# Kernel tuning notes

Measured on AMD Instinct MI355X. Metric: run time of the kernel, lower is better.

The kernel has to match this reference:

```python
import jax, jax.numpy as jnp
import numpy as np

LAM = 20.0      # Sinkhorn entropic sharpness (exp(-LAM*M))
N_ITERS = 20    # fixed Sinkhorn iterations
EPS = 1e-8


def setup_inputs() -> dict:
    key = jax.random.key(0)
    k1, k2, k3, k4 = jax.random.split(key, 4)
    n, l, h, hid = 16, 256, 128, 128
    f = jax.random.normal(k1, (n, l, l, h), dtype=jnp.float32) * 0.1
    head = jax.random.uniform(k2, (n, l, l), dtype=jnp.float32)
    W1 = jax.random.normal(k3, (h, hid), dtype=jnp.float32) * (1.0 / np.sqrt(h))
    b1 = jnp.zeros((hid,), dtype=jnp.float32)
    W2 = jax.random.normal(k4, (hid, 1), dtype=jnp.float32) * (1.0 / np.sqrt(hid))
    b2 = jnp.zeros((1,), dtype=jnp.float32)
    return {"f": f, "head": head, "W1": W1, "b1": b1, "W2": W2, "b2": b2}


def _sinkhorn_loss(r, c, M):
    # r, c: (l,) histograms; M: (l, l) ground cost. Frogner-style Wasserstein loss.
    K = jnp.exp(-LAM * M)
    KM = K * M
    u0 = jnp.full_like(r, 1.0 / r.shape[0])

    def body(u, _):
        u = r / (K @ (c / (K.T @ u + EPS)) + EPS)
        return u, None

    u, _ = jax.lax.scan(body, u0, None, length=N_ITERS)
    v = c / (K.T @ u + EPS)
    return jnp.sum(u * (KM @ v))


def reference(f, head, W1, b1, W2, b2):
    n, l, _, h = f.shape
    # dense 2-layer MLP over every (i,j) arc feature -> scalar score
    hdn = jnp.tanh(f.reshape(n, l * l, h) @ W1 + b1)          # (n, l*l, hid)
    scores = (hdn @ W2 + b2).reshape(n, l, l)                  # (n, l, l)
    # per-sample ground cost: elementwise f * f^T reduced over feature dim
    C = jnp.einsum('nijh,njih->nij', f, f)                     # (n, l, l)
    Cn = C / (jnp.max(jnp.abs(C), axis=(1, 2), keepdims=True) + EPS)
    preds = scores + EPS
    targets = head + EPS
    r = jax.nn.softmax(preds, axis=-1)                         # rows as pred histograms
    c = targets / jnp.sum(targets, axis=-1, keepdims=True)
    # vmap over batch, then over rows; cost shared across rows of a sample
    per_row = jax.vmap(jax.vmap(_sinkhorn_loss, in_axes=(0, 0, None)),
                       in_axes=(0, 0, 0))(r, c, Cn)            # (n, l)
    wloss = jnp.sum(per_row)
    return scores, wloss
```

## Files before the change

### kernel.cpp

```cpp
#include <hip/hip_runtime.h>
#include <math.h>

#define NB 16
#define L 256
#define H 128
#define HID 128
#define LAMF 20.0f
#define EPSF 1e-8f
#define NITER 20

#define GLL16(gp, lp) __builtin_amdgcn_global_load_lds( \
    (const __attribute__((address_space(1))) unsigned int*)(gp), \
    (__attribute__((address_space(3))) unsigned int*)(lp), 16, 0, 0)
#define WAITVM2() __builtin_amdgcn_s_waitcnt(0x0F72)
#define WAITVM0() __builtin_amdgcn_s_waitcnt(0x0F70)
#define WAITLGKM0() __builtin_amdgcn_s_waitcnt(0xC07F)

__global__ __launch_bounds__(256) void k_scores(
    const float* __restrict__ f, const float* __restrict__ W1,
    const float* __restrict__ b1, const float* __restrict__ W2,
    const float* __restrict__ b2, float* __restrict__ scores)
{
    __shared__ float As[32][68];
    __shared__ float Bs[32][132];
    const int tid = threadIdx.x;
    const int tx = tid & 31;
    const int ty = tid >> 5;
    const long m0 = (long)blockIdx.x * 64;

    float acc[8][4];
#pragma unroll
    for (int i = 0; i < 8; i++)
#pragma unroll
        for (int c = 0; c < 4; c++) acc[i][c] = 0.f;

    for (int kc = 0; kc < H; kc += 32) {
        {
            const int k = tid & 31, mb = tid >> 5;
#pragma unroll
            for (int r = 0; r < 8; r++) {
                int m = mb + r * 8;
                As[k][m] = f[(m0 + m) * H + kc + k];
            }
        }
        {
#pragma unroll
            for (int r = 0; r < 16; r++) {
                int idx = r * 256 + tid;
                int k = idx >> 7, n = idx & 127;
                Bs[k][n] = W1[(kc + k) * HID + n];
            }
        }
        __syncthreads();
#pragma unroll
        for (int k = 0; k < 32; k++) {
            float4 a0 = *(const float4*)&As[k][ty * 8];
            float4 a1 = *(const float4*)&As[k][ty * 8 + 4];
            float4 bv = *(const float4*)&Bs[k][tx * 4];
            float av[8] = {a0.x, a0.y, a0.z, a0.w, a1.x, a1.y, a1.z, a1.w};
            float bb[4] = {bv.x, bv.y, bv.z, bv.w};
#pragma unroll
            for (int i = 0; i < 8; i++)
#pragma unroll
                for (int c = 0; c < 4; c++)
                    acc[i][c] = fmaf(av[i], bb[c], acc[i][c]);
        }
        __syncthreads();
    }
    float part[8];
#pragma unroll
    for (int i = 0; i < 8; i++) part[i] = 0.f;
#pragma unroll
    for (int c = 0; c < 4; c++) {
        int col = tx * 4 + c;
        float b1v = b1[col], w2v = W2[col];
#pragma unroll
        for (int i = 0; i < 8; i++) {
            float hv = tanhf(acc[i][c] + b1v);
            part[i] = fmaf(hv, w2v, part[i]);
        }
    }
#pragma unroll
    for (int off = 16; off >= 1; off >>= 1)
#pragma unroll
        for (int i = 0; i < 8; i++)
            part[i] += __shfl_xor(part[i], off, 64);
    if (tx == 0) {
        float b2v = b2[0];
#pragma unroll
        for (int i = 0; i < 8; i++) {
            int row = ty * 8 + i;
            scores[m0 + row] = part[i] + b2v;
        }
    }
}

__global__ __launch_bounds__(256) void k_cost(
    const float* __restrict__ f, float* __restrict__ C)
{
    const int bid = blockIdx.x;
    const int s = bid >> 8, i = bid & 255;
    const int wave = threadIdx.x >> 6, lane = threadIdx.x & 63;
    const long base_i = ((long)(s * L + i)) * L;
    for (int j4 = i; j4 < L; j4 += 4) {
        int j = j4 + wave;
        if (j < L) {
            const float2 x = *(const float2*)&f[(base_i + j) * (long)H + lane * 2];
            const float2 y = *(const float2*)&f[(((long)(s * L + j)) * L + i) * (long)H + lane * 2];
            float d = fmaf(x.x, y.x, x.y * y.y);
#pragma unroll
            for (int off = 32; off >= 1; off >>= 1) d += __shfl_xor(d, off, 64);
            if (lane == 0) {
                C[base_i + j] = d;
                C[((long)(s * L + j)) * L + i] = d;
            }
        }
    }
}

__global__ __launch_bounds__(256) void k_absmax(
    const float* __restrict__ C, float* __restrict__ maxabs)
{
    __shared__ float red[256];
    const int s = blockIdx.x, tid = threadIdx.x;
    const float* Cp = C + (long)s * L * L;
    float m = 0.f;
    for (int idx = tid; idx < L * L; idx += 256) m = fmaxf(m, fabsf(Cp[idx]));
    red[tid] = m;
    __syncthreads();
    for (int o = 128; o >= 1; o >>= 1) {
        if (tid < o) red[tid] = fmaxf(red[tid], red[tid + o]);
        __syncthreads();
    }
    if (tid == 0) maxabs[s] = red[0];
}

__global__ __launch_bounds__(512) void k_kmat(
    const float* __restrict__ C, const float* __restrict__ maxabs,
    float* __restrict__ Km, float* __restrict__ KMm)
{
    long idx = (long)blockIdx.x * blockDim.x + threadIdx.x;
    const long tot = (long)NB * L * L;
    for (; idx < tot; idx += (long)gridDim.x * blockDim.x) {
        int s = (int)(idx >> 16);
        float cn = C[idx] / (maxabs[s] + EPSF);
        float kv = __expf(-LAMF * cn);
        Km[idx] = kv;
        KMm[idx] = kv * cn;
    }
}

__global__ __launch_bounds__(256) void k_rc(
    const float* __restrict__ scores, const float* __restrict__ head,
    float* __restrict__ R, float* __restrict__ Cd)
{
    __shared__ float red[256];
    const long base = (long)blockIdx.x * L;
    const int t = threadIdx.x;
    float sc = scores[base + t];
    red[t] = sc;
    __syncthreads();
    for (int o = 128; o >= 1; o >>= 1) {
        if (t < o) red[t] = fmaxf(red[t], red[t + o]);
        __syncthreads();
    }
    float mx = red[0];
    __syncthreads();
    float e = __expf(sc - mx);
    red[t] = e;
    __syncthreads();
    for (int o = 128; o >= 1; o >>= 1) {
        if (t < o) red[t] += red[t + o];
        __syncthreads();
    }
    float es = red[0];
    __syncthreads();
    R[base + t] = e / es;
    float hv = head[base + t] + EPSF;
    red[t] = hv;
    __syncthreads();
    for (int o = 128; o >= 1; o >>= 1) {
        if (t < o) red[t] += red[t + o];
        __syncthreads();
    }
    float hs = red[0];
    Cd[base + t] = hv / hs;
}

__global__ __launch_bounds__(512) void k_sink(
    const float* __restrict__ Km, const float* __restrict__ KMm,
    const float* __restrict__ R, const float* __restrict__ Cd,
    float* __restrict__ lossbuf)
{
    __shared__ __align__(128) float Kw[8 * 2 * 512];
    __shared__ __align__(128) float Uc[4096];
    __shared__ __align__(128) float Tc[4096];

    const int bid = blockIdx.x;
    const int s = bid >> 4;
    const int j0 = (bid & 15) * 16;
    const float* Kp  = Km  + (long)s * 65536;
    const float* KMp = KMm + (long)s * 65536;
    const float* Rp  = R  + (long)s * 65536 + (long)j0 * L;
    const float* Cp  = Cd + (long)s * 65536 + (long)j0 * L;

    const int tid  = threadIdx.x;
    const int w    = tid >> 6;
    const int lane = tid & 63;
    const int ta   = lane & 7;
    const int jh   = lane >> 3;
    const int ab   = w * 32 + ta * 4;
    const int jb   = jh * 2;

    const int o0 = lane * 16;
    const int o1 = (64 + lane) * 16;
    char* lbase = (char*)&Kw[w * 1024];
    const int gcol = w * 128;

    const float4 cva = *(const float4*)&Cp[jb * L + ab];
    const float4 cvb = *(const float4*)&Cp[(jb + 1) * L + ab];
    const float4 rva = *(const float4*)&Rp[jb * L + ab];
    const float4 rvb = *(const float4*)&Rp[(jb + 1) * L + ab];
    const float ca[4] = {cva.x, cva.y, cva.z, cva.w};
    const float cb[4] = {cvb.x, cvb.y, cvb.z, cvb.w};
    const float ra[4] = {rva.x, rva.y, rva.z, rva.w};
    const float rb[4] = {rvb.x, rvb.y, rvb.z, rvb.w};

    for (int idx = tid; idx < 4096; idx += 512) Uc[idx] = 1.0f / L;
    __syncthreads();

    float acc[4][2];

    auto stage = [&](const float* Mg, int b0, int buf) {
        const char* g = (const char*)Mg + (size_t)b0 * 1024 + gcol;
        char* l = lbase + (buf << 11);
        GLL16(g + ((o0 >> 7) << 10) + (o0 & 127), l + o0);
        GLL16(g + ((o1 >> 7) << 10) + (o1 & 127), l + o1);
    };

    auto run_pass = [&](const float* __restrict__ Mg, const float* __restrict__ S) {
#pragma unroll
        for (int ai = 0; ai < 4; ai++) { acc[ai][0] = 0.f; acc[ai][1] = 0.f; }
        stage(Mg, 0, 0);
        for (int t = 0; t < 16; t++) {
            WAITLGKM0();
            if (t < 15) {
                stage(Mg, (t + 1) * 16, (t + 1) & 1);
                WAITVM2();
            } else {
                WAITVM0();
            }
            const float* Kb = &Kw[w * 1024 + ((t & 1) << 9)] + ta * 4;
            const float* St = S + (t << 8);
#pragma unroll
            for (int bbi = 0; bbi < 16; bbi++) {
                float4 kv = *(const float4*)&Kb[bbi * 32];
                float2 sv = *(const float2*)&St[bbi * 16 + (jb ^ (bbi & 14))];
                acc[0][0] = fmaf(kv.x, sv.x, acc[0][0]); acc[0][1] = fmaf(kv.x, sv.y, acc[0][1]);
                acc[1][0] = fmaf(kv.y, sv.x, acc[1][0]); acc[1][1] = fmaf(kv.y, sv.y, acc[1][1]);
                acc[2][0] = fmaf(kv.z, sv.x, acc[2][0]); acc[2][1] = fmaf(kv.z, sv.y, acc[2][1]);
                acc[3][0] = fmaf(kv.w, sv.x, acc[3][0]); acc[3][1] = fmaf(kv.w, sv.y, acc[3][1]);
            }
        }
    };

    float lp = 0.f;
    for (int it = 0; it < NITER; it++) {
        run_pass(Kp, Uc);
#pragma unroll
        for (int ai = 0; ai < 4; ai++) {
            const int bI = ab + ai;
            float2 o;
            o.x = ca[ai] / (acc[ai][0] + EPSF);
            o.y = cb[ai] / (acc[ai][1] + EPSF);
            *(float2*)&Tc[bI * 16 + (jb ^ (bI & 14))] = o;
        }
        __syncthreads();
        run_pass(Kp, Tc);
#pragma unroll
        for (int ai = 0; ai < 4; ai++) {
            const int bI = ab + ai;
            float2 o;
            o.x = ra[ai] / (acc[ai][0] + EPSF);
            o.y = rb[ai] / (acc[ai][1] + EPSF);
            *(float2*)&Uc[bI * 16 + (jb ^ (bI & 14))] = o;
        }
        __syncthreads();
    }
    run_pass(Kp, Uc);
#pragma unroll
    for (int ai = 0; ai < 4; ai++) {
        const int bI = ab + ai;
        float2 o;
        o.x = ca[ai] / (acc[ai][0] + EPSF);
        o.y = cb[ai] / (acc[ai][1] + EPSF);
        *(float2*)&Tc[bI * 16 + (jb ^ (bI & 14))] = o;
    }
    __syncthreads();
    run_pass(KMp, Tc);
#pragma unroll
    for (int ai = 0; ai < 4; ai++) {
        const int bI = ab + ai;
#pragma unroll
        for (int cj = 0; cj < 2; cj++)
            lp += Uc[bI * 16 + ((jb + cj) ^ (bI & 14))] * acc[ai][cj];
    }
    __syncthreads();
    float* red = Kw;
    red[tid] = lp;
    __syncthreads();
    for (int o = 256; o >= 1; o >>= 1) {
        if (tid < o) red[tid] += red[tid + o];
        __syncthreads();
    }
    if (tid == 0) lossbuf[bid] = red[0];
}

__global__ __launch_bounds__(256) void k_final(
    const float* __restrict__ lossbuf, float* __restrict__ out)
{
    __shared__ float red[256];
    int t = threadIdx.x;
    red[t] = lossbuf[t];
    __syncthreads();
    for (int o = 128; o >= 1; o >>= 1) {
        if (t < o) red[t] += red[t + o];
        __syncthreads();
    }
    if (t == 0) out[0] = red[0];
}

extern "C" void kernel_launch(void* const* d_in, const int* in_sizes, int n_in,
                              void* d_out, int out_size, void* d_ws, size_t ws_size,
                              hipStream_t stream)
{
    const float* f    = (const float*)d_in[0];
    const float* head = (const float*)d_in[1];
    const float* W1   = (const float*)d_in[2];
    const float* b1   = (const float*)d_in[3];
    const float* W2   = (const float*)d_in[4];
    const float* b2   = (const float*)d_in[5];
    float* scores = (float*)d_out;
    float* wloss  = scores + (long)NB * L * L;

    float* ws      = (float*)d_ws;
    float* C       = ws;
    float* Km      = ws + 1 * 1048576;
    float* KMm     = ws + 2 * 1048576;
    float* R       = ws + 3 * 1048576;
    float* Cd      = ws + 4 * 1048576;
    float* maxabs  = ws + 5 * 1048576;
    float* lossbuf = maxabs + 64;

    k_scores<<<16384, 256, 0, stream>>>(f, W1, b1, W2, b2, scores);
    k_cost  <<<4096,  256, 0, stream>>>(f, C);
    k_absmax<<<NB,    256, 0, stream>>>(C, maxabs);
    k_kmat  <<<2048,  512, 0, stream>>>(C, maxabs, Km, KMm);
    k_rc    <<<NB * L, 256, 0, stream>>>(scores, head, R, Cd);
    k_sink  <<<NB * 16, 512, 0, stream>>>(Km, KMm, R, Cd, lossbuf);
    k_final <<<1, 256, 0, stream>>>(lossbuf, wloss);
}
```

Before: 1.727 ms.

## Retile Sinkhorn matvec to 4x4 register blocks with split-K across wave halves

Restructures the Sinkhorn K-matvec tiling so each thread computes a 4x4 (rows x columns) register tile instead of 4x2. The reduction dimension is split between two halves of the waves, with partial sums combined through a new shared buffer before the update. Staging now uses larger chunks (8 steps of 4 loads) and padded stride-20 vector layouts replace the XOR swizzle. This raises FMA-per-load reuse and cuts LDS traffic per FMA, at the cost of an extra shared-memory reduction and barrier per pass, plus more LDS use.

```diff
diff --git a/kernel.cpp b/kernel.cpp
--- a/kernel.cpp
+++ b/kernel.cpp
@@ -12,7 +12,7 @@
 #define GLL16(gp, lp) __builtin_amdgcn_global_load_lds( \
     (const __attribute__((address_space(1))) unsigned int*)(gp), \
     (__attribute__((address_space(3))) unsigned int*)(lp), 16, 0, 0)
-#define WAITVM2() __builtin_amdgcn_s_waitcnt(0x0F72)
+#define WAITVM4() __builtin_amdgcn_s_waitcnt(0x0F74)
 #define WAITVM0() __builtin_amdgcn_s_waitcnt(0x0F70)
 #define WAITLGKM0() __builtin_amdgcn_s_waitcnt(0xC07F)
 
@@ -192,128 +192,157 @@
     const float* __restrict__ R, const float* __restrict__ Cd,
     float* __restrict__ lossbuf)
 {
-    __shared__ __align__(128) float Kw[8 * 2 * 512];
-    __shared__ __align__(128) float Uc[4096];
-    __shared__ __align__(128) float Tc[4096];
+    __shared__ __align__(128) float Kw[16384];
+    __shared__ __align__(128) float Uc[5120];
+    __shared__ __align__(128) float Tc[5120];
+    __shared__ __align__(128) float Sc[5120];
 
     const int bid = blockIdx.x;
     const int s = bid >> 4;
     const int j0 = (bid & 15) * 16;
-    const float* Kp  = Km  + (long)s * 65536;
-    const float* KMp = KMm + (long)s * 65536;
+    const char* Kpb  = (const char*)(Km  + (long)s * 65536);
+    const char* KMpb = (const char*)(KMm + (long)s * 65536);
     const float* Rp  = R  + (long)s * 65536 + (long)j0 * L;
     const float* Cp  = Cd + (long)s * 65536 + (long)j0 * L;
 
     const int tid  = threadIdx.x;
     const int w    = tid >> 6;
     const int lane = tid & 63;
-    const int ta   = lane & 7;
-    const int jh   = lane >> 3;
-    const int ab   = w * 32 + ta * 4;
-    const int jb   = jh * 2;
-
-    const int o0 = lane * 16;
-    const int o1 = (64 + lane) * 16;
-    char* lbase = (char*)&Kw[w * 1024];
-    const int gcol = w * 128;
-
-    const float4 cva = *(const float4*)&Cp[jb * L + ab];
-    const float4 cvb = *(const float4*)&Cp[(jb + 1) * L + ab];
-    const float4 rva = *(const float4*)&Rp[jb * L + ab];
-    const float4 rvb = *(const float4*)&Rp[(jb + 1) * L + ab];
-    const float ca[4] = {cva.x, cva.y, cva.z, cva.w};
-    const float cb[4] = {cvb.x, cvb.y, cvb.z, cvb.w};
-    const float ra[4] = {rva.x, rva.y, rva.z, rva.w};
-    const float rb[4] = {rvb.x, rvb.y, rvb.z, rvb.w};
-
-    for (int idx = tid; idx < 4096; idx += 512) Uc[idx] = 1.0f / L;
-    __syncthreads();
-
-    float acc[4][2];
-
-    auto stage = [&](const float* Mg, int b0, int buf) {
-        const char* g = (const char*)Mg + (size_t)b0 * 1024 + gcol;
-        char* l = lbase + (buf << 11);
-        GLL16(g + ((o0 >> 7) << 10) + (o0 & 127), l + o0);
-        GLL16(g + ((o1 >> 7) << 10) + (o1 & 127), l + o1);
+    const int ag   = w & 3;
+    const int bh   = w >> 2;
+    const int ta   = lane & 15;
+    const int jq   = lane >> 4;
+    const int a_base = ag * 64 + ta * 4;
+    const int j_base = jq * 4;
+
+    const int glane = (bh * 128 + jq) * 1024 + ag * 256 + ta * 16;
+    char* const ldst = (char*)Kw + w * 8192 + lane * 16;
+
+    float cc[4][4], rr[4][4];
+    if (bh == 0) {
+#pragma unroll
+        for (int ji = 0; ji < 4; ji++) {
+            float4 cv = *(const float4*)&Cp[(j_base + ji) * L + a_base];
+            float4 rv = *(const float4*)&Rp[(j_base + ji) * L + a_base];
+            cc[ji][0] = cv.x; cc[ji][1] = cv.y; cc[ji][2] = cv.z; cc[ji][3] = cv.w;
+            rr[ji][0] = rv.x; rr[ji][1] = rv.y; rr[ji][2] = rv.z; rr[ji][3] = rv.w;
+        }
+    }
+
+    for (int idx = tid; idx < 5120; idx += 512) Uc[idx] = 1.0f / L;
+    __syncthreads();
+
+    float acc[4][4];
+
+    auto stage = [&](const char* Mgb, int t, int buf) {
+        const char* g = Mgb + glane + t * 16384;
+        char* l = ldst + (buf << 12);
+        GLL16(g,         l);
+        GLL16(g + 4096,  l + 1024);
+        GLL16(g + 8192,  l + 2048);
+        GLL16(g + 12288, l + 3072);
     };
 
-    auto run_pass = [&](const float* __restrict__ Mg, const float* __restrict__ S) {
-#pragma unroll
-        for (int ai = 0; ai < 4; ai++) { acc[ai][0] = 0.f; acc[ai][1] = 0.f; }
-        stage(Mg, 0, 0);
-        for (int t = 0; t < 16; t++) {
+    auto run_pass = [&](const char* __restrict__ Mgb, const float* __restrict__ S) {
+#pragma unroll
+        for (int ai = 0; ai < 4; ai++)
+#pragma unroll
+            for (int ji = 0; ji < 4; ji++) acc[ai][ji] = 0.f;
+        stage(Mgb, 0, 0);
+        const float* Sj = S + 4 * jq;
+        for (int t = 0; t < 8; t++) {
             WAITLGKM0();
-            if (t < 15) {
-                stage(Mg, (t + 1) * 16, (t + 1) & 1);
-                WAITVM2();
+            if (t < 7) {
+                stage(Mgb, t + 1, (t + 1) & 1);
+                WAITVM4();
             } else {
                 WAITVM0();
             }
-            const float* Kb = &Kw[w * 1024 + ((t & 1) << 9)] + ta * 4;
-            const float* St = S + (t << 8);
+            const float* Kt = Kw + w * 2048 + ((t & 1) << 10) + ta * 4;
+            const float* St = Sj + (bh * 128 + t * 16) * 20;
 #pragma unroll
             for (int bbi = 0; bbi < 16; bbi++) {
-                float4 kv = *(const float4*)&Kb[bbi * 32];
-                float2 sv = *(const float2*)&St[bbi * 16 + (jb ^ (bbi & 14))];
-                acc[0][0] = fmaf(kv.x, sv.x, acc[0][0]); acc[0][1] = fmaf(kv.x, sv.y, acc[0][1]);
-                acc[1][0] = fmaf(kv.y, sv.x, acc[1][0]); acc[1][1] = fmaf(kv.y, sv.y, acc[1][1]);
-                acc[2][0] = fmaf(kv.z, sv.x, acc[2][0]); acc[2][1] = fmaf(kv.z, sv.y, acc[2][1]);
-                acc[3][0] = fmaf(kv.w, sv.x, acc[3][0]); acc[3][1] = fmaf(kv.w, sv.y, acc[3][1]);
+                float4 kv = *(const float4*)(Kt + bbi * 64);
+                float4 sv = *(const float4*)(St + bbi * 20);
+                float kk[4] = {kv.x, kv.y, kv.z, kv.w};
+                float ss[4] = {sv.x, sv.y, sv.z, sv.w};
+#pragma unroll
+                for (int ai = 0; ai < 4; ai++)
+#pragma unroll
+                    for (int ji = 0; ji < 4; ji++)
+                        acc[ai][ji] = fmaf(kk[ai], ss[ji], acc[ai][ji]);
             }
         }
     };
 
+    const int slot = (ag * 64 + lane) * 20;
+
+    auto reduce_update = [&](float* __restrict__ dst, const float (*cr)[4]) {
+        if (bh == 1) {
+#pragma unroll
+            for (int ai = 0; ai < 4; ai++) {
+                float4 o;
+                o.x = acc[ai][0]; o.y = acc[ai][1]; o.z = acc[ai][2]; o.w = acc[ai][3];
+                *(float4*)&Sc[slot + 4 * ai] = o;
+            }
+        }
+        __syncthreads();
+        if (bh == 0) {
+#pragma unroll
+            for (int ai = 0; ai < 4; ai++) {
+                float4 p = *(const float4*)&Sc[slot + 4 * ai];
+                float s0 = acc[ai][0] + p.x;
+                float s1 = acc[ai][1] + p.y;
+                float s2 = acc[ai][2] + p.z;
+                float s3 = acc[ai][3] + p.w;
+                float4 o;
+                o.x = cr[0][ai] / (s0 + EPSF);
+                o.y = cr[1][ai] / (s1 + EPSF);
+                o.z = cr[2][ai] / (s2 + EPSF);
+                o.w = cr[3][ai] / (s3 + EPSF);
+                *(float4*)&dst[(a_base + ai) * 20 + j_base] = o;
+            }
+        }
+        __syncthreads();
+    };
+
+    for (int it = 0; it < NITER; it++) {
+        run_pass(Kpb, Uc);
+        reduce_update(Tc, cc);
+        run_pass(Kpb, Tc);
+        reduce_update(Uc, rr);
+    }
+    run_pass(Kpb, Uc);
+    reduce_update(Tc, cc);
+    run_pass(KMpb, Tc);
     float lp = 0.f;
-    for (int it = 0; it < NITER; it++) {
-        run_pass(Kp, Uc);
+    if (bh == 1) {
 #pragma unroll
         for (int ai = 0; ai < 4; ai++) {
-            const int bI = ab + ai;
-            float2 o;
-            o.x = ca[ai] / (acc[ai][0] + EPSF);
-            o.y = cb[ai] / (acc[ai][1] + EPSF);
-            *(float2*)&Tc[bI * 16 + (jb ^ (bI & 14))] = o;
-        }
-        __syncthreads();
-        run_pass(Kp, Tc);
+            float4 o;
+            o.x = acc[ai][0]; o.y = acc[ai][1]; o.z = acc[ai][2]; o.w = acc[ai][3];
+            *(float4*)&Sc[slot + 4 * ai] = o;
+        }
+    }
+    __syncthreads();
+    if (bh == 0) {
 #pragma unroll
         for (int ai = 0; ai < 4; ai++) {
-            const int bI = ab + ai;
-            float2 o;
-            o.x = ra[ai] / (acc[ai][0] + EPSF);
-            o.y = rb[ai] / (acc[ai][1] + EPSF);
-            *(float2*)&Uc[bI * 16 + (jb ^ (bI & 14))] = o;
-        }
-        __syncthreads();
-    }
-    run_pass(Kp, Uc);
-#pragma unroll
-    for (int ai = 0; ai < 4; ai++) {
-        const int bI = ab + ai;
-        float2 o;
-        o.x = ca[ai] / (acc[ai][0] + EPSF);
-        o.y = cb[ai] / (acc[ai][1] + EPSF);
-        *(float2*)&Tc[bI * 16 + (jb ^ (bI & 14))] = o;
-    }
-    __syncthreads();
-    run_pass(KMp, Tc);
-#pragma unroll
-    for (int ai = 0; ai < 4; ai++) {
-        const int bI = ab + ai;
-#pragma unroll
-        for (int cj = 0; cj < 2; cj++)
-            lp += Uc[bI * 16 + ((jb + cj) ^ (bI & 14))] * acc[ai][cj];
-    }
-    __syncthreads();
-    float* red = Kw;
-    red[tid] = lp;
+            float4 p = *(const float4*)&Sc[slot + 4 * ai];
+            float4 u = *(const float4*)&Uc[(a_base + ai) * 20 + j_base];
+            lp += u.x * (acc[ai][0] + p.x);
+            lp += u.y * (acc[ai][1] + p.y);
+            lp += u.z * (acc[ai][2] + p.z);
+            lp += u.w * (acc[ai][3] + p.w);
+        }
+    }
+    Tc[tid] = lp;
     __syncthreads();
     for (int o = 256; o >= 1; o >>= 1) {
-        if (tid < o) red[tid] += red[tid + o];
-        __syncthreads();
-    }
-    if (tid == 0) lossbuf[bid] = red[0];
+        if (tid < o) Tc[tid] += Tc[tid + o];
+        __syncthreads();
+    }
+    if (tid == 0) lossbuf[bid] = Tc[0];
 }
 
 __global__ __launch_bounds__(256) void k_final(
```

After: 1.596 ms. -7.6%, faster.
